# Kernel optimization log

Measured on AMD Instinct MI355X. Metric: run time of the kernel, lower is better.

## Reference

```python
import jax, jax.numpy as jnp
import numpy as np

WAY = 5
SHOT = 5
TUPLES = 56          # C(8,3)
D_IN = 6144          # trans_linear_in_dim * temporal_set_size
D_OUT = 1024         # trans_linear_in_dim // 2
N_Q = 100
N_S = WAY * SHOT


def setup_inputs() -> dict:
    key = jax.random.key(0)
    k1, k2, k3, k4 = jax.random.split(key, 4)
    support_set = jax.random.normal(k1, (N_S, TUPLES, D_IN), dtype=jnp.float32)
    queries = jax.random.normal(k2, (N_Q, TUPLES, D_IN), dtype=jnp.float32)
    # 5-way 5-shot labels, each class present SHOT times
    support_labels = (jnp.arange(N_S) % WAY).astype(jnp.int64)
    clsW_w = jax.random.normal(k3, (D_OUT, D_IN), dtype=jnp.float32) * (1.0 / np.sqrt(D_IN))
    clsW_b = jax.random.normal(k4, (D_OUT,), dtype=jnp.float32) * 0.01
    return {"support_set": support_set, "support_labels": support_labels,
            "queries": queries, "clsW_w": clsW_w, "clsW_b": clsW_b}


def reference(support_set, support_labels, queries, clsW_w, clsW_b):
    n_q, T, d_in = queries.shape
    # query projection + relu: [n_q*T, D_OUT]  (dropout omitted: eval-mode determinism)
    q = jax.nn.relu(queries.reshape(-1, d_in) @ clsW_w.T + clsW_b)
    q_sq = jnp.sum(q * q, axis=1)  # [n_q*T]

    # per-class support row indices (fixed SHOT per class -> jit-safe nonzero)
    def class_idx(c):
        return jnp.nonzero(support_labels == c, size=SHOT, fill_value=0)[0]
    idxs = jax.vmap(class_idx)(jnp.arange(WAY))  # [WAY, SHOT]

    def per_class(idx):
        s = support_set[idx].reshape(-1, d_in)             # [SHOT*T, D_IN]
        se = jax.nn.relu(s @ clsW_w.T + clsW_b)            # [SHOT*T, D_OUT]
        s_sq = jnp.sum(se * se, axis=1)                    # [SHOT*T]
        # euclidean cdist via quadratic expansion
        d2 = q_sq[:, None] + s_sq[None, :] - 2.0 * (q @ se.T)
        d = jnp.sqrt(jnp.maximum(d2, 0.0))                 # [n_q*T, SHOT*T]
        min_dist = d.min(axis=1).reshape(n_q, T)           # [n_q, T]
        return -min_dist.mean(axis=1)                      # [n_q]

    dist_all = jax.vmap(per_class)(idxs).T  # [n_q, WAY]
    return dist_all
```

## Files before the change

kernel.cpp:

```cpp
#include <hip/hip_runtime.h>
#include <hip/hip_bf16.h>
#include <stdint.h>

#define WAY   5
#define TUP   56
#define DIN   6144
#define DOUT  1024
#define NQ    100
#define MQ    5600
#define MS    1400
#define MX    7000
#define INFB  0x7F800000
#define KSPLIT 2
#define KSEG  (DIN / KSPLIT)
#define NT    (KSEG / 64)

typedef __attribute__((ext_vector_type(8))) short  short8;
typedef __attribute__((ext_vector_type(4))) float  f32x4;
typedef __attribute__((ext_vector_type(4))) unsigned int u32x4;

__device__ __forceinline__ unsigned short f2bf(float f) {
  unsigned u = __float_as_uint(f);
  u += 0x7FFFu + ((u >> 16) & 1u);
  return (unsigned short)(u >> 16);
}
__device__ __forceinline__ float bf2f(unsigned short h) {
  return __uint_as_float(((unsigned)h) << 16);
}

#define GLOAD16(gp, lp)                                                              \
  __builtin_amdgcn_global_load_lds((__attribute__((address_space(1))) void*)(gp),    \
                                   (__attribute__((address_space(3))) void*)(lp),    \
                                   16, 0, 0)

#define SB0()        __builtin_amdgcn_sched_barrier(0)
#define MEMPIN()     do { asm volatile("" ::: "memory"); SB0(); } while (0)
#define S_BARRIER()  asm volatile("s_barrier" ::: "memory")
#define LGKM0()      do { SB0(); asm volatile("s_waitcnt lgkmcnt(0)" ::: "memory"); SB0(); } while (0)
#define LGKM(n)      do { SB0(); asm volatile("s_waitcnt lgkmcnt(" #n ")" ::: "memory"); SB0(); } while (0)
#define VMCNT(n)     do { SB0(); asm volatile("s_waitcnt vmcnt(" #n ")" ::: "memory"); SB0(); } while (0)

__global__ void convW_init(const float* __restrict__ wsrc,
                           unsigned short* __restrict__ Wb,
                           int* __restrict__ mbits) {
  const int UW = DOUT * (DIN / 8);
  int gtid = blockIdx.x * blockDim.x + threadIdx.x;
  int stride = gridDim.x * blockDim.x;
  if (gtid < MQ * WAY) mbits[gtid] = INFB;
  for (int u = gtid; u < UW; u += stride) {
    const float* src = wsrc + (size_t)u * 8;
    f32x4 a = *(const f32x4*)src;
    f32x4 b = *(const f32x4*)(src + 4);
    short8 p;
    p[0] = (short)f2bf(a[0]); p[1] = (short)f2bf(a[1]);
    p[2] = (short)f2bf(a[2]); p[3] = (short)f2bf(a[3]);
    p[4] = (short)f2bf(b[0]); p[5] = (short)f2bf(b[1]);
    p[6] = (short)f2bf(b[2]); p[7] = (short)f2bf(b[3]);
    *(short8*)&Wb[(size_t)u * 8] = p;
  }
}

__device__ __forceinline__ void stage_op64(const unsigned short* __restrict__ g,
                                           int ldk, int rowBaseG, int rowMax,
                                           int k0, unsigned short* ldsTile,
                                           int opRow0, int tid) {
  int r  = opRow0 + (tid >> 3);
  int ks = (tid & 7) ^ (r & 7);
  int grow = rowBaseG + r; if (grow > rowMax) grow = rowMax;
  const unsigned short* gp = g + (size_t)grow * ldk + k0 + (ks << 3);
  unsigned short* lp = ldsTile + opRow0 * 64 + ((tid & ~63) << 3);
  GLOAD16(gp, lp);
}

__device__ __forceinline__ void issueA(const float* __restrict__ qsrc,
                                       const float* __restrict__ ssrc,
                                       int rowBase, int k0, int tid, f32x4 (&aR)[8]) {
  int rt = tid >> 3;
  int cf = k0 + (tid & 7) * 8;
  #pragma unroll
  for (int c = 0; c < 4; ++c) {
    int grow = rowBase + rt + c * 64;
    if (grow > MX - 1) grow = MX - 1;
    const float* src = (grow < MQ) ? (qsrc + (size_t)grow * DIN + cf)
                                   : (ssrc + (size_t)(grow - MQ) * DIN + cf);
    aR[c * 2]     = *(const f32x4*)(src);
    aR[c * 2 + 1] = *(const f32x4*)(src + 4);
  }
}

__device__ __forceinline__ void writeA(unsigned short* An, int tid, const f32x4 (&aR)[8]) {
  int rt = tid >> 3;
  int sp = (tid & 7) ^ (rt & 7);
  #pragma unroll
  for (int c = 0; c < 4; ++c) {
    u32x4 w;
    #pragma unroll
    for (int j = 0; j < 2; ++j) {
      const f32x4 v = aR[c * 2 + j];
      __hip_bfloat162 h0 = __float22bfloat162_rn(make_float2(v[0], v[1]));
      __hip_bfloat162 h1 = __float22bfloat162_rn(make_float2(v[2], v[3]));
      w[j * 2]     = *(const unsigned int*)&h0;
      w[j * 2 + 1] = *(const unsigned int*)&h1;
    }
    *(u32x4*)(An + (rt + c * 64) * 64 + sp * 8) = w;
  }
}

#define MFMA16(ACCR, BSEL)                                                               \
  __builtin_amdgcn_s_setprio(1);                                                         \
  _Pragma("unroll")                                                                      \
  for (int f = 0; f < 4; ++f) {                                                          \
    _Pragma("unroll")                                                                    \
    for (int n = 0; n < 2; ++n) {                                                        \
      acc[ACCR][BSEL * 2 + n] = __builtin_amdgcn_mfma_f32_16x16x32_bf16(                 \
          a[f][0], B_##BSEL[n][0], acc[ACCR][BSEL * 2 + n], 0, 0, 0);                    \
      acc[ACCR][BSEL * 2 + n] = __builtin_amdgcn_mfma_f32_16x16x32_bf16(                 \
          a[f][1], B_##BSEL[n][1], acc[ACCR][BSEL * 2 + n], 0, 0, 0);                    \
    }                                                                                    \
  }                                                                                      \
  __builtin_amdgcn_s_setprio(0);

__device__ __forceinline__ void do_tile(
    const unsigned short* __restrict__ Ac, const unsigned short* __restrict__ Bc,
    unsigned short* An, unsigned short* Bn,
    const float* __restrict__ qsrc, const float* __restrict__ ssrc,
    const unsigned short* __restrict__ Wb,
    int rowBase, int colBase, int kB, int kA, int tid,
    int wrB, int wcB, int l15, int sw0, int sw1,
    f32x4 (&aR)[8],
    short8 (&a)[4][2], short8 (&B_0)[2][2], short8 (&B_1)[2][2], f32x4 (&acc)[8][4]) {
  #pragma unroll
  for (int f = 0; f < 4; ++f) {
    int r = (wrB + f * 16 + l15) * 64;
    a[f][0] = *(const short8*)&Ac[r + sw0];
    a[f][1] = *(const short8*)&Ac[r + sw1];
  }
  #pragma unroll
  for (int n = 0; n < 2; ++n) {
    int r = (wcB + n * 16 + l15) * 64;
    B_0[n][0] = *(const short8*)&Bc[r + sw0];
    B_0[n][1] = *(const short8*)&Bc[r + sw1];
  }
  MEMPIN();
  #pragma unroll
  for (int n = 0; n < 2; ++n) {
    int r = (wcB + (n + 2) * 16 + l15) * 64;
    B_1[n][0] = *(const short8*)&Bc[r + sw0];
    B_1[n][1] = *(const short8*)&Bc[r + sw1];
  }
  MEMPIN();
  stage_op64(Wb, DIN, colBase, DOUT - 1, kB, Bn, 0,  tid);
  stage_op64(Wb, DIN, colBase, DOUT - 1, kB, Bn, 64, tid);
  LGKM(4);
  MFMA16(f, 0)
  MEMPIN();
  stage_op64(Wb, DIN, colBase, DOUT - 1, kB, Bn, 128, tid);
  stage_op64(Wb, DIN, colBase, DOUT - 1, kB, Bn, 192, tid);
  LGKM0();
  MFMA16(f, 1)
  MEMPIN();
  #pragma unroll
  for (int f = 0; f < 4; ++f) {
    int r = (wrB + (f + 4) * 16 + l15) * 64;
    a[f][0] = *(const short8*)&Ac[r + sw0];
    a[f][1] = *(const short8*)&Ac[r + sw1];
  }
  VMCNT(4);
  writeA(An, tid, aR);
  MEMPIN();
  issueA(qsrc, ssrc, rowBase, kA, tid, aR);
  LGKM(4);
  MFMA16(f + 4, 1)
  MEMPIN();
  MFMA16(f + 4, 0)
  LGKM0();
  VMCNT(8);
  S_BARRIER(); SB0();
}

__launch_bounds__(512, 2)
__global__ void gemm1_8ph(const float* __restrict__ qsrc,
                          const float* __restrict__ ssrc,
                          const unsigned short* __restrict__ Wb,
                          unsigned short* __restrict__ Cp) {
  __shared__ __align__(16) unsigned short As[2][256 * 64];
  __shared__ __align__(16) unsigned short Bs[2][256 * 64];
  const int tid  = threadIdx.x;
  const int lane = tid & 63;
  const int wid  = tid >> 6;
  const int wr = wid >> 2, wc = wid & 3;
  const int l15 = lane & 15, l16 = lane >> 4, l7 = lane & 7;
  const int wrB = wr * 128, wcB = wc * 64;
  const int sw0 = ((l16) ^ l7) << 3;
  const int sw1 = ((4 + l16) ^ l7) << 3;

  const int id = blockIdx.x;
  const int c  = id & 7;
  const int q  = id >> 3;
  const int nIdx = q & 3;
  const int g  = (q >> 2) * 8 + c;
  const int mIdx  = g % 28;
  const int split = g / 28;

  const int rowBase = mIdx * 256;
  const int colBase = nIdx * 256;
  const int kBeg = split * KSEG;
  unsigned short* Cout = Cp + (size_t)split * MX * DOUT;

  f32x4 acc[8][4];
  #pragma unroll
  for (int f = 0; f < 8; ++f)
    #pragma unroll
    for (int n = 0; n < 4; ++n) acc[f][n] = (f32x4){0.f, 0.f, 0.f, 0.f};

  f32x4 aR[8];
  issueA(qsrc, ssrc, rowBase, kBeg, tid, aR);
  SB0();
  stage_op64(Wb, DIN, colBase, DOUT - 1, kBeg, Bs[0], 0,   tid);
  stage_op64(Wb, DIN, colBase, DOUT - 1, kBeg, Bs[0], 64,  tid);
  stage_op64(Wb, DIN, colBase, DOUT - 1, kBeg, Bs[0], 128, tid);
  stage_op64(Wb, DIN, colBase, DOUT - 1, kBeg, Bs[0], 192, tid);
  VMCNT(4);
  writeA(As[0], tid, aR);
  issueA(qsrc, ssrc, rowBase, kBeg + 64, tid, aR);
  LGKM0();
  VMCNT(8);
  S_BARRIER(); SB0();

  short8 a[4][2], B_0[2][2], B_1[2][2];

  for (int T = 0; T < NT; T += 2) {
    int kB1 = kBeg + ((T + 1 < NT) ? (T + 1) : (NT - 1)) * 64;
    int kA1 = kBeg + ((T + 2 < NT) ? (T + 2) : (NT - 1)) * 64;
    do_tile(As[0], Bs[0], As[1], Bs[1], qsrc, ssrc, Wb, rowBase, colBase,
            kB1, kA1, tid, wrB, wcB, l15, sw0, sw1, aR, a, B_0, B_1, acc);
    int kB2 = kBeg + ((T + 2 < NT) ? (T + 2) : (NT - 1)) * 64;
    int kA2 = kBeg + ((T + 3 < NT) ? (T + 3) : (NT - 1)) * 64;
    do_tile(As[1], Bs[1], As[0], Bs[0], qsrc, ssrc, Wb, rowBase, colBase,
            kB2, kA2, tid, wrB, wcB, l15, sw0, sw1, aR, a, B_0, B_1, acc);
  }
  asm volatile("s_waitcnt vmcnt(0)" ::: "memory");

  #pragma unroll
  for (int f = 0; f < 8; ++f)
    #pragma unroll
    for (int r = 0; r < 4; ++r) {
      int row = rowBase + wrB + f * 16 + l16 * 4 + r;
      if (row < MX) {
        size_t rb = (size_t)row * DOUT + colBase + wcB + l15;
        #pragma unroll
        for (int n = 0; n < 4; ++n)
          Cout[rb + n * 16] = f2bf(acc[f][n][r]);
      }
    }
}

__launch_bounds__(256, 8)
__global__ void epi_kernel(const unsigned short* __restrict__ Cp,
                           const float* __restrict__ bias,
                           unsigned short* __restrict__ E,
                           float* __restrict__ sq) {
  __shared__ float part[4];
  int tid = threadIdx.x;
  int half = tid >> 7;
  int t    = tid & 127;
  int row  = blockIdx.x * 2 + half;
  size_t base = (size_t)row * DOUT + t * 8;

  float v[8];
  #pragma unroll
  for (int j = 0; j < 8; ++j) v[j] = 0.f;
  #pragma unroll
  for (int s = 0; s < KSPLIT; ++s) {
    short8 p = *(const short8*)&Cp[(size_t)s * MX * DOUT + base];
    #pragma unroll
    for (int j = 0; j < 8; ++j) v[j] += bf2f((unsigned short)p[j]);
  }
  f32x4 b0 = *(const f32x4*)&bias[t * 8];
  f32x4 b1 = *(const f32x4*)&bias[t * 8 + 4];
  float ss = 0.f;
  short8 e;
  #pragma unroll
  for (int j = 0; j < 8; ++j) {
    float w = v[j] + (j < 4 ? b0[j] : b1[j - 4]);
    w = fmaxf(w, 0.f);
    unsigned short h = f2bf(w);
    e[j] = (short)h;
    float wb = bf2f(h);
    ss += wb * wb;
  }
  *(short8*)&E[base] = e;
  #pragma unroll
  for (int off = 1; off < 64; off <<= 1) ss += __shfl_xor(ss, off, 64);
  if ((tid & 63) == 0) part[tid >> 6] = ss;
  __syncthreads();
  if (t == 0) sq[row] = part[half * 2] + part[half * 2 + 1];
}

__device__ __forceinline__ void stage128x64(const unsigned short* __restrict__ g,
                                            int ldk, int rowBase, int rowMax, int k0,
                                            unsigned short* lds, int tid) {
  int wbase = tid & ~63;
  #pragma unroll
  for (int li = 0; li < 4; ++li) {
    int flat = li * 256 + tid;
    int r  = flat >> 3;
    int s  = flat & 7;
    int ks = s ^ (r & 7);
    int grow = rowBase + r;
    if (grow > rowMax) grow = rowMax;
    const unsigned short* gp = g + (size_t)grow * ldk + k0 + (ks << 3);
    unsigned short* lp = lds + ((li * 256 + wbase) << 3);
    GLOAD16(gp, lp);
  }
}

__launch_bounds__(256, 2)
__global__ void gemm2_kernel(const unsigned short* __restrict__ E,
                             const float* __restrict__ sq,
                             int* __restrict__ mbits) {
  __shared__ __align__(16) unsigned short As[2][128 * 64];
  __shared__ __align__(16) unsigned short Bs[2][128 * 64];
  int tid = threadIdx.x;
  int lane = tid & 63, wid = tid >> 6;
  int wr = wid >> 1, wc = wid & 1;

  const int id  = blockIdx.x;
  const int xcd = id & 7;
  const int pos = id >> 3;
  const int f   = (xcd < 4) ? (xcd * 61 + pos) : (244 + (xcd - 4) * 60 + pos);
  const int rowBase = (f / 11) * 128;
  const int colBase = (f % 11) * 128;

  const unsigned short* Aq = E;
  const unsigned short* Bsup = E + (size_t)MQ * DOUT;

  f32x4 acc[4][4];
  #pragma unroll
  for (int m = 0; m < 4; ++m)
    #pragma unroll
    for (int n = 0; n < 4; ++n) acc[m][n] = (f32x4){0.f, 0.f, 0.f, 0.f};

  stage128x64(Aq, DOUT, rowBase, MQ - 1, 0, As[0], tid);
  stage128x64(Bsup, DOUT, colBase, MS - 1, 0, Bs[0], tid);
  VMCNT(0);
  S_BARRIER(); SB0();

  int cur = 0;
  const int NK = DOUT / 64;
  for (int t = 0; t < NK; ++t) {
    int kn = ((t + 1 < NK) ? (t + 1) : t) * 64;
    stage128x64(Aq, DOUT, rowBase, MQ - 1, kn, As[cur ^ 1], tid);
    stage128x64(Bsup, DOUT, colBase, MS - 1, kn, Bs[cur ^ 1], tid);
    const unsigned short* Ac = As[cur];
    const unsigned short* Bc = Bs[cur];
    #pragma unroll
    for (int h = 0; h < 2; ++h) {
      short8 af[4], bfr[4];
      int ks = (h << 2) + (lane >> 4);
      int sw = ((ks ^ (lane & 7)) << 3);
      #pragma unroll
      for (int m = 0; m < 4; ++m) {
        int ra = wr * 64 + m * 16 + (lane & 15);
        af[m] = *(const short8*)&Ac[ra * 64 + sw];
      }
      #pragma unroll
      for (int n = 0; n < 4; ++n) {
        int rb = wc * 64 + n * 16 + (lane & 15);
        bfr[n] = *(const short8*)&Bs[cur][rb * 64 + sw];
        (void)Bc;
      }
      #pragma unroll
      for (int m = 0; m < 4; ++m)
        #pragma unroll
        for (int n = 0; n < 4; ++n)
          acc[m][n] = __builtin_amdgcn_mfma_f32_16x16x32_bf16(af[m], bfr[n], acc[m][n], 0, 0, 0);
    }
    VMCNT(0);
    LGKM0();
    S_BARRIER(); SB0();
    cur ^= 1;
  }

  int* mlds = (int*)As;
  for (int i = tid; i < 128 * WAY; i += 256) mlds[i] = INFB;
  __syncthreads();

  float ssqv[4]; int cls[4]; int jcol[4];
  #pragma unroll
  for (int n = 0; n < 4; ++n) {
    int j = colBase + wc * 64 + n * 16 + (lane & 15);
    jcol[n] = j;
    if (j < MS) { ssqv[n] = sq[MQ + j]; cls[n] = (j / TUP) % WAY; }
    else        { ssqv[n] = 0.f;        cls[n] = 0; }
  }

  #pragma unroll
  for (int m = 0; m < 4; ++m) {
    #pragma unroll
    for (int r = 0; r < 4; ++r) {
      int rit  = wr * 64 + m * 16 + (lane >> 4) * 4 + r;
      int grow = rowBase + rit;
      if (grow < MQ) {
        float qs = sq[grow];
        #pragma unroll
        for (int n = 0; n < 4; ++n) {
          if (jcol[n] < MS) {
            float d2 = fmaxf(qs + ssqv[n] - 2.f * acc[m][n][r], 0.f);
            atomicMin(&mlds[rit * WAY + cls[n]], __float_as_int(d2));
          }
        }
      }
    }
  }
  __syncthreads();
  for (int i = tid; i < 128 * WAY; i += 256) {
    int rit = i / WAY, c2 = i - rit * WAY;
    int grow = rowBase + rit;
    int v = mlds[i];
    if (grow < MQ && v != INFB) atomicMin(&mbits[grow * WAY + c2], v);
  }
}

__global__ void final_kernel(const int* __restrict__ mbits, float* __restrict__ out) {
  int tid = blockIdx.x * blockDim.x + threadIdx.x;
  if (tid < NQ * WAY) {
    int qi = tid / WAY, c = tid % WAY;
    float s = 0.f;
    for (int t = 0; t < TUP; ++t)
      s += sqrtf(__int_as_float(mbits[(qi * TUP + t) * WAY + c]));
    out[tid] = -s * (1.f / TUP);
  }
}

extern "C" void kernel_launch(void* const* d_in, const int* in_sizes, int n_in,
                              void* d_out, int out_size, void* d_ws, size_t ws_size,
                              hipStream_t stream) {
  const float* support = (const float*)d_in[0];
  const float* queries = (const float*)d_in[2];
  const float* W       = (const float*)d_in[3];
  const float* bvec    = (const float*)d_in[4];
  float* out = (float*)d_out;

  char* ws = (char*)d_ws;
  unsigned short* Wb = (unsigned short*)(ws);
  unsigned short* E  = (unsigned short*)(ws + 12582912);
  float* sq          = (float*)(ws + 26918912);
  int*   mbits       = (int*)(ws + 26947072);
  unsigned short* Cp = (unsigned short*)(ws + 27059200);

  convW_init<<<dim3(2048), dim3(256), 0, stream>>>(W, Wb, mbits);
  gemm1_8ph<<<dim3(224), dim3(512), 0, stream>>>(queries, support, Wb, Cp);
  epi_kernel<<<dim3(MX / 2), dim3(256), 0, stream>>>(Cp, bvec, E, sq);
  gemm2_kernel<<<dim3(484), dim3(256), 0, stream>>>(E, sq, mbits);
  final_kernel<<<dim3(2), dim3(256), 0, stream>>>(mbits, out);
}
```

Before: 141.7 us.

## Load GEMM1 weight fragments directly from global into registers, dropping LDS staging

The first GEMM stopped staging the bf16 weight (B) tile through LDS with global_load_lds. Each wave now reads its own MFMA B fragments straight from global memory into registers, using precomputed per-lane row offsets. This removes half the LDS footprint and the LDS write/read traffic for B, and the pipeline waits are reordered around the new loads. In exchange, B reuse across the two wave rows now depends on the cache rather than LDS, and global-load latency sits directly ahead of the MFMAs, with less double-buffered prefetch lead time.

```diff
diff --git a/kernel.cpp b/kernel.cpp
--- a/kernel.cpp
+++ b/kernel.cpp
@@ -37,7 +37,6 @@
 #define MEMPIN()     do { asm volatile("" ::: "memory"); SB0(); } while (0)
 #define S_BARRIER()  asm volatile("s_barrier" ::: "memory")
 #define LGKM0()      do { SB0(); asm volatile("s_waitcnt lgkmcnt(0)" ::: "memory"); SB0(); } while (0)
-#define LGKM(n)      do { SB0(); asm volatile("s_waitcnt lgkmcnt(" #n ")" ::: "memory"); SB0(); } while (0)
 #define VMCNT(n)     do { SB0(); asm volatile("s_waitcnt vmcnt(" #n ")" ::: "memory"); SB0(); } while (0)
 
 __global__ void convW_init(const float* __restrict__ wsrc,
@@ -60,18 +59,6 @@
   }
 }
 
-__device__ __forceinline__ void stage_op64(const unsigned short* __restrict__ g,
-                                           int ldk, int rowBaseG, int rowMax,
-                                           int k0, unsigned short* ldsTile,
-                                           int opRow0, int tid) {
-  int r  = opRow0 + (tid >> 3);
-  int ks = (tid & 7) ^ (r & 7);
-  int grow = rowBaseG + r; if (grow > rowMax) grow = rowMax;
-  const unsigned short* gp = g + (size_t)grow * ldk + k0 + (ks << 3);
-  unsigned short* lp = ldsTile + opRow0 * 64 + ((tid & ~63) << 3);
-  GLOAD16(gp, lp);
-}
-
 __device__ __forceinline__ void issueA(const float* __restrict__ qsrc,
                                        const float* __restrict__ ssrc,
                                        int rowBase, int k0, int tid, f32x4 (&aR)[8]) {
@@ -121,60 +108,51 @@
   __builtin_amdgcn_s_setprio(0);
 
 __device__ __forceinline__ void do_tile(
-    const unsigned short* __restrict__ Ac, const unsigned short* __restrict__ Bc,
-    unsigned short* An, unsigned short* Bn,
+    const unsigned short* __restrict__ Ac, unsigned short* An,
     const float* __restrict__ qsrc, const float* __restrict__ ssrc,
-    const unsigned short* __restrict__ Wb,
-    int rowBase, int colBase, int kB, int kA, int tid,
-    int wrB, int wcB, int l15, int sw0, int sw1,
+    const unsigned short* __restrict__ Wb, const unsigned bOff[4],
+    int rowBase, int kT, int kA, int tid,
+    int wrB, int l15, int l16, int sw0, int sw1,
     f32x4 (&aR)[8],
     short8 (&a)[4][2], short8 (&B_0)[2][2], short8 (&B_1)[2][2], f32x4 (&acc)[8][4]) {
+  writeA(An, tid, aR);
+  MEMPIN();
+  #pragma unroll
+  for (int n = 0; n < 2; ++n) {
+    const unsigned short* bp = Wb + bOff[n] + kT;
+    B_0[n][0] = *(const short8*)(bp + l16 * 8);
+    B_0[n][1] = *(const short8*)(bp + 32 + l16 * 8);
+  }
+  MEMPIN();
+  #pragma unroll
+  for (int n = 0; n < 2; ++n) {
+    const unsigned short* bp = Wb + bOff[n + 2] + kT;
+    B_1[n][0] = *(const short8*)(bp + l16 * 8);
+    B_1[n][1] = *(const short8*)(bp + 32 + l16 * 8);
+  }
+  MEMPIN();
+  issueA(qsrc, ssrc, rowBase, kA, tid, aR);
+  MEMPIN();
   #pragma unroll
   for (int f = 0; f < 4; ++f) {
     int r = (wrB + f * 16 + l15) * 64;
     a[f][0] = *(const short8*)&Ac[r + sw0];
     a[f][1] = *(const short8*)&Ac[r + sw1];
   }
-  #pragma unroll
-  for (int n = 0; n < 2; ++n) {
-    int r = (wcB + n * 16 + l15) * 64;
-    B_0[n][0] = *(const short8*)&Bc[r + sw0];
-    B_0[n][1] = *(const short8*)&Bc[r + sw1];
-  }
-  MEMPIN();
-  #pragma unroll
-  for (int n = 0; n < 2; ++n) {
-    int r = (wcB + (n + 2) * 16 + l15) * 64;
-    B_1[n][0] = *(const short8*)&Bc[r + sw0];
-    B_1[n][1] = *(const short8*)&Bc[r + sw1];
-  }
-  MEMPIN();
-  stage_op64(Wb, DIN, colBase, DOUT - 1, kB, Bn, 0,  tid);
-  stage_op64(Wb, DIN, colBase, DOUT - 1, kB, Bn, 64, tid);
-  LGKM(4);
+  LGKM0();
+  VMCNT(12);
   MFMA16(f, 0)
-  MEMPIN();
-  stage_op64(Wb, DIN, colBase, DOUT - 1, kB, Bn, 128, tid);
-  stage_op64(Wb, DIN, colBase, DOUT - 1, kB, Bn, 192, tid);
-  LGKM0();
+  VMCNT(8);
   MFMA16(f, 1)
-  MEMPIN();
   #pragma unroll
   for (int f = 0; f < 4; ++f) {
     int r = (wrB + (f + 4) * 16 + l15) * 64;
     a[f][0] = *(const short8*)&Ac[r + sw0];
     a[f][1] = *(const short8*)&Ac[r + sw1];
   }
-  VMCNT(4);
-  writeA(An, tid, aR);
-  MEMPIN();
-  issueA(qsrc, ssrc, rowBase, kA, tid, aR);
-  LGKM(4);
+  LGKM0();
   MFMA16(f + 4, 1)
-  MEMPIN();
   MFMA16(f + 4, 0)
-  LGKM0();
-  VMCNT(8);
   S_BARRIER(); SB0();
 }
 
@@ -184,7 +162,6 @@
                           const unsigned short* __restrict__ Wb,
                           unsigned short* __restrict__ Cp) {
   __shared__ __align__(16) unsigned short As[2][256 * 64];
-  __shared__ __align__(16) unsigned short Bs[2][256 * 64];
   const int tid  = threadIdx.x;
   const int lane = tid & 63;
   const int wid  = tid >> 6;
@@ -207,6 +184,11 @@
   const int kBeg = split * KSEG;
   unsigned short* Cout = Cp + (size_t)split * MX * DOUT;
 
+  unsigned bOff[4];
+  #pragma unroll
+  for (int n = 0; n < 4; ++n)
+    bOff[n] = (unsigned)(colBase + wcB + n * 16 + l15) * DIN + kBeg;
+
   f32x4 acc[8][4];
   #pragma unroll
   for (int f = 0; f < 8; ++f)
@@ -215,29 +197,24 @@
 
   f32x4 aR[8];
   issueA(qsrc, ssrc, rowBase, kBeg, tid, aR);
-  SB0();
-  stage_op64(Wb, DIN, colBase, DOUT - 1, kBeg, Bs[0], 0,   tid);
-  stage_op64(Wb, DIN, colBase, DOUT - 1, kBeg, Bs[0], 64,  tid);
-  stage_op64(Wb, DIN, colBase, DOUT - 1, kBeg, Bs[0], 128, tid);
-  stage_op64(Wb, DIN, colBase, DOUT - 1, kBeg, Bs[0], 192, tid);
-  VMCNT(4);
+  MEMPIN();
   writeA(As[0], tid, aR);
+  MEMPIN();
   issueA(qsrc, ssrc, rowBase, kBeg + 64, tid, aR);
   LGKM0();
-  VMCNT(8);
   S_BARRIER(); SB0();
 
   short8 a[4][2], B_0[2][2], B_1[2][2];
 
   for (int T = 0; T < NT; T += 2) {
-    int kB1 = kBeg + ((T + 1 < NT) ? (T + 1) : (NT - 1)) * 64;
-    int kA1 = kBeg + ((T + 2 < NT) ? (T + 2) : (NT - 1)) * 64;
-    do_tile(As[0], Bs[0], As[1], Bs[1], qsrc, ssrc, Wb, rowBase, colBase,
-            kB1, kA1, tid, wrB, wcB, l15, sw0, sw1, aR, a, B_0, B_1, acc);
-    int kB2 = kBeg + ((T + 2 < NT) ? (T + 2) : (NT - 1)) * 64;
-    int kA2 = kBeg + ((T + 3 < NT) ? (T + 3) : (NT - 1)) * 64;
-    do_tile(As[1], Bs[1], As[0], Bs[0], qsrc, ssrc, Wb, rowBase, colBase,
-            kB2, kA2, tid, wrB, wcB, l15, sw0, sw1, aR, a, B_0, B_1, acc);
+    int kT1 = T * 64;
+    int kA1 = ((T + 2 < NT) ? (T + 2) : (NT - 1)) * 64 + kBeg;
+    do_tile(As[0], As[1], qsrc, ssrc, Wb, bOff, rowBase, kT1, kA1,
+            tid, wrB, l15, l16, sw0, sw1, aR, a, B_0, B_1, acc);
+    int kT2 = (T + 1) * 64;
+    int kA2 = ((T + 3 < NT) ? (T + 3) : (NT - 1)) * 64 + kBeg;
+    do_tile(As[1], As[0], qsrc, ssrc, Wb, bOff, rowBase, kT2, kA2,
+            tid, wrB, l15, l16, sw0, sw1, aR, a, B_0, B_1, acc);
   }
   asm volatile("s_waitcnt vmcnt(0)" ::: "memory");
 
@@ -319,8 +296,8 @@
 __global__ void gemm2_kernel(const unsigned short* __restrict__ E,
                              const float* __restrict__ sq,
                              int* __restrict__ mbits) {
-  __shared__ __align__(16) unsigned short As[2][128 * 64];
-  __shared__ __align__(16) unsigned short Bs[2][128 * 64];
+  __shared__ __align__(16) unsigned short As2[2][128 * 64];
+  __shared__ __align__(16) unsigned short Bs2[2][128 * 64];
   int tid = threadIdx.x;
   int lane = tid & 63, wid = tid >> 6;
   int wr = wid >> 1, wc = wid & 1;
@@ -341,19 +318,20 @@
     #pragma unroll
     for (int n = 0; n < 4; ++n) acc[m][n] = (f32x4){0.f, 0.f, 0.f, 0.f};
 
-  stage128x64(Aq, DOUT, rowBase, MQ - 1, 0, As[0], tid);
-  stage128x64(Bsup, DOUT, colBase, MS - 1, 0, Bs[0], tid);
-  VMCNT(0);
+  stage128x64(Aq, DOUT, rowBase, MQ - 1, 0, As2[0], tid);
+  stage128x64(Bsup, DOUT, colBase, MS - 1, 0, Bs2[0], tid);
+  asm volatile("s_waitcnt vmcnt(0)" ::: "memory");
+  SB0();
   S_BARRIER(); SB0();
 
   int cur = 0;
   const int NK = DOUT / 64;
   for (int t = 0; t < NK; ++t) {
     int kn = ((t + 1 < NK) ? (t + 1) : t) * 64;
-    stage128x64(Aq, DOUT, rowBase, MQ - 1, kn, As[cur ^ 1], tid);
-    stage128x64(Bsup, DOUT, colBase, MS - 1, kn, Bs[cur ^ 1], tid);
-    const unsigned short* Ac = As[cur];
-    const unsigned short* Bc = Bs[cur];
+    stage128x64(Aq, DOUT, rowBase, MQ - 1, kn, As2[cur ^ 1], tid);
+    stage128x64(Bsup, DOUT, colBase, MS - 1, kn, Bs2[cur ^ 1], tid);
+    const unsigned short* Ac = As2[cur];
+    const unsigned short* Bc = Bs2[cur];
     #pragma unroll
     for (int h = 0; h < 2; ++h) {
       short8 af[4], bfr[4];
@@ -367,8 +345,7 @@
       #pragma unroll
       for (int n = 0; n < 4; ++n) {
         int rb = wc * 64 + n * 16 + (lane & 15);
-        bfr[n] = *(const short8*)&Bs[cur][rb * 64 + sw];
-        (void)Bc;
+        bfr[n] = *(const short8*)&Bc[rb * 64 + sw];
       }
       #pragma unroll
       for (int m = 0; m < 4; ++m)
@@ -376,13 +353,14 @@
         for (int n = 0; n < 4; ++n)
           acc[m][n] = __builtin_amdgcn_mfma_f32_16x16x32_bf16(af[m], bfr[n], acc[m][n], 0, 0, 0);
     }
-    VMCNT(0);
-    LGKM0();
+    asm volatile("s_waitcnt vmcnt(0)" ::: "memory");
+    asm volatile("s_waitcnt lgkmcnt(0)" ::: "memory");
+    SB0();
     S_BARRIER(); SB0();
     cur ^= 1;
   }
 
-  int* mlds = (int*)As;
+  int* mlds = (int*)As2;
   for (int i = tid; i < 128 * WAY; i += 256) mlds[i] = INFB;
   __syncthreads();
 
```

Result: slower. 208.4 us (+47.0%).
